# Performance work log

Measured on AMD Instinct MI355X. Metric: run time of the kernel, lower is better.

## Reference

```python
import jax, jax.numpy as jnp
import numpy as np

H, L, NB = 128, 2048, 64  # features, seq len, half state size (conj-symmetric N=128)


def _forward(u, x_re, x_im, Lambda_re, Lambda_im, B_re, B_im, C_re, C_im, D, d):
    Lam = (Lambda_re + 1j * Lambda_im).astype(jnp.complex64)   # (H, NB) discrete diag A
    B = (B_re + 1j * B_im).astype(jnp.complex64)               # (H, NB)
    C = (C_re + 1j * C_im).astype(jnp.complex64)               # (H, NB)
    x0 = (x_re + 1j * x_im).astype(jnp.complex64)              # (H, NB) initial state
    Hn, Ln = u.shape
    # scan elements (A_t, b_t, d_t); identity element (1, x0, False) prepended at t=0
    A = jnp.concatenate([jnp.ones((Hn, 1, NB), jnp.complex64),
                         jnp.broadcast_to(Lam[:, None, :], (Hn, Ln, NB))], axis=1)
    b = jnp.concatenate([x0[:, None, :],
                         B[:, None, :] * u[:, :, None].astype(jnp.complex64)], axis=1)
    dd = jnp.concatenate([jnp.zeros((1,), bool), d.astype(bool)])[None, :, None]  # (1, L+1, 1)

    def combine(lhs, rhs):
        # reset-aware associative combine: if right done-flag set, drop left contribution
        A_i, b_i, c_i = lhs
        A_j, b_j, c_j = rhs
        return (jnp.where(c_j, A_j, A_j * A_i),
                jnp.where(c_j, b_j, A_j * b_i + b_j),
                jnp.logical_or(c_i, c_j))

    _, xs, _ = jax.lax.associative_scan(combine, (A, b, dd), axis=1)
    xs = xs[:, 1:]                                             # (H, L, NB) hidden states
    # conj symmetry: y_t = 2*Re(C @ x_t) + D * u_t
    y = 2.0 * jnp.real(jnp.einsum('hn,hln->hl', C, xs)) + D[:, None] * u
    return y, xs[:, -1]


def setup_inputs():
    key = jax.random.key(0)
    ks = jax.random.split(key, 8)
    # stable ZOH-discretized HiPPO-like diagonal system (mirrors LSSL-f init)
    dts = jnp.logspace(-3.0, -1.0, H)                          # (H,) per-feature timescales
    k = jnp.arange(NB, dtype=jnp.float32)
    lam_c = -0.5 + 1j * jnp.pi * (2.0 * k + 1.0)               # (NB,) continuous poles
    lam_d = jnp.exp(dts[:, None] * lam_c[None, :]).astype(jnp.complex64)  # (H, NB), |.|<1
    Bc = ((jax.random.normal(ks[0], (NB,)) + 1j * jax.random.normal(ks[1], (NB,)))
          / jnp.sqrt(2.0 * NB)).astype(jnp.complex64)
    Bd = (((lam_d - 1.0) / lam_c[None, :]) * Bc[None, :]).astype(jnp.complex64)  # (H, NB)
    C = ((jax.random.normal(ks[2], (H, NB)) + 1j * jax.random.normal(ks[3], (H, NB)))
         / jnp.sqrt(float(NB))).astype(jnp.complex64)
    return {
        "u": jax.random.normal(ks[4], (H, L), jnp.float32),
        "x_re": jnp.zeros((H, NB), jnp.float32),
        "x_im": jnp.zeros((H, NB), jnp.float32),
        "Lambda_re": jnp.real(lam_d).astype(jnp.float32),
        "Lambda_im": jnp.imag(lam_d).astype(jnp.float32),
        "B_re": jnp.real(Bd).astype(jnp.float32),
        "B_im": jnp.imag(Bd).astype(jnp.float32),
        "C_re": jnp.real(C).astype(jnp.float32),
        "C_im": jnp.imag(C).astype(jnp.float32),
        "D": jax.random.normal(ks[5], (H,), jnp.float32),
        "d": jax.random.bernoulli(ks[6], 0.01, (L,)),
    }


def reference(u, x_re, x_im, Lambda_re, Lambda_im, B_re, B_im, C_re, C_im, D, d):
    return _forward(u, x_re, x_im, Lambda_re, Lambda_im, B_re, B_im, C_re, C_im, D, d)
```

## Files before the change

### kernel.cpp

```cpp
#include <hip/hip_runtime.h>

#define Hn 128
#define Ln 2048
#define NBn 64
#define K 64
#define G 32
#define PITCH 65

__global__ __launch_bounds__(64) void phase1_local(
    const float* __restrict__ u,
    const float* __restrict__ Lre,  const float* __restrict__ Lim,
    const float* __restrict__ Bre,  const float* __restrict__ Bim,
    const float* __restrict__ Cre,  const float* __restrict__ Cim,
    const float* __restrict__ Dv,   const int* __restrict__ dflag,
    float* __restrict__ out,
    float* __restrict__ Acr, float* __restrict__ Aci,
    float* __restrict__ Bcr, float* __restrict__ Bci)
{
    __shared__ float g_s[K * PITCH];
    __shared__ float u_s[K];
    __shared__ int   d_s[K];

    const int g = blockIdx.x, h = blockIdx.y, n = threadIdx.x;
    const int hn = h * NBn + n;
    const int l0 = g * K;

    const float lre = Lre[hn], lim = Lim[hn];
    const float bre = Bre[hn], bim = Bim[hn];
    const float c2re =  2.0f * Cre[hn];
    const float c2im = -2.0f * Cim[hn];
    const float Dh   = Dv[h];

    u_s[n] = u[h * Ln + l0 + n];
    const int dn = dflag[l0 + n];
    d_s[n] = dn;
    __syncthreads();

    float zre = 0.f, zim = 0.f;
    #pragma unroll
    for (int k = 0; k < K; ++k) {
        const float ul = u_s[k];
        const bool  rs = d_s[k] != 0;
        const float bur = bre * ul;
        const float bui = bim * ul;
        const float tre = fmaf(lre, zre, fmaf(-lim, zim, bur));
        const float tim = fmaf(lre, zim, fmaf( lim, zre, bui));
        zre = rs ? bur : tre;
        zim = rs ? bui : tim;
        g_s[k * PITCH + n] = fmaf(c2re, zre, c2im * zim);
    }
    __syncthreads();

    const float* row = g_s + n * PITCH;
    float a0 = 0.f, a1 = 0.f, a2 = 0.f, a3 = 0.f;
    #pragma unroll
    for (int k = 0; k < NBn; k += 4) {
        a0 += row[k + 0]; a1 += row[k + 1];
        a2 += row[k + 2]; a3 += row[k + 3];
    }
    out[h * Ln + l0 + n] = (a0 + a1) + (a2 + a3) + Dh * u_s[n];

    const unsigned long long bal = __ballot(dn != 0);
    float pr = lre, pi = lim;
    #pragma unroll
    for (int it = 0; it < 6; ++it) {
        const float nr = pr * pr - pi * pi;
        const float ni = 2.f * pr * pi;
        pr = nr; pi = ni;
    }
    if (bal) { pr = 0.f; pi = 0.f; }
    const int idx = (h * G + g) * NBn + n;
    Acr[idx] = pr;  Aci[idx] = pi;
    Bcr[idx] = zre; Bci[idx] = zim;
}

__global__ __launch_bounds__(64) void phase2_combine(
    const float* __restrict__ x_re, const float* __restrict__ x_im,
    const float* __restrict__ Acr,  const float* __restrict__ Aci,
    float* __restrict__ Bcr,        float* __restrict__ Bci,
    float* __restrict__ out)
{
    const int h = blockIdx.x, n = threadIdx.x;
    const int hn = h * NBn + n;
    float sre = x_re[hn], sim = x_im[hn];
    #pragma unroll
    for (int g = 0; g < G; ++g) {
        const int idx = (h * G + g) * NBn + n;
        const float ar = Acr[idx], ai = Aci[idx];
        const float br = Bcr[idx], bi = Bci[idx];
        Bcr[idx] = sre;
        Bci[idx] = sim;
        const float nr = fmaf(ar, sre, fmaf(-ai, sim, br));
        const float ni = fmaf(ar, sim, fmaf( ai, sre, bi));
        sre = nr; sim = ni;
    }
    float* xlast = out + Hn * Ln;
    xlast[2 * hn + 0] = sre;
    xlast[2 * hn + 1] = sim;
}

__global__ __launch_bounds__(64) void phase3_fixup(
    const float* __restrict__ Lre, const float* __restrict__ Lim,
    const float* __restrict__ Cre, const float* __restrict__ Cim,
    const int* __restrict__ dflag,
    const float* __restrict__ Scr, const float* __restrict__ Sci,
    float* __restrict__ out)
{
    __shared__ float g_s[K * PITCH];

    const int g = blockIdx.x, h = blockIdx.y, n = threadIdx.x;
    const int hn = h * NBn + n;
    const int l0 = g * K;
    const int idx = (h * G + g) * NBn + n;

    const float sr = Scr[idx], si = Sci[idx];
    const float cr = Cre[hn],  ci = Cim[hn];
    const float lre = Lre[hn], lim = Lim[hn];

    float tr = cr * sr - ci * si;
    float ti = cr * si + ci * sr;

    const int dn = dflag[l0 + n];
    const unsigned long long bal = __ballot(dn != 0);
    const int kr = bal ? (__ffsll(bal) - 1) : K;

    #pragma unroll
    for (int k = 0; k < K; ++k) {
        const float nr = fmaf(lre, tr, -lim * ti);
        const float ni = fmaf(lre, ti,  lim * tr);
        tr = nr; ti = ni;
        g_s[k * PITCH + n] = tr;
    }
    __syncthreads();

    const float* row = g_s + n * PITCH;
    float a0 = 0.f, a1 = 0.f, a2 = 0.f, a3 = 0.f;
    #pragma unroll
    for (int k = 0; k < NBn; k += 4) {
        a0 += row[k + 0]; a1 += row[k + 1];
        a2 += row[k + 2]; a3 += row[k + 3];
    }
    if (n < kr)
        out[h * Ln + l0 + n] += 2.f * ((a0 + a1) + (a2 + a3));
}

extern "C" void kernel_launch(void* const* d_in, const int* in_sizes, int n_in,
                              void* d_out, int out_size, void* d_ws, size_t ws_size,
                              hipStream_t stream) {
    const float* u    = (const float*)d_in[0];
    const float* x_re = (const float*)d_in[1];
    const float* x_im = (const float*)d_in[2];
    const float* Lre  = (const float*)d_in[3];
    const float* Lim  = (const float*)d_in[4];
    const float* Bre  = (const float*)d_in[5];
    const float* Bim  = (const float*)d_in[6];
    const float* Cre  = (const float*)d_in[7];
    const float* Cim  = (const float*)d_in[8];
    const float* Dv   = (const float*)d_in[9];
    const int*   dfl  = (const int*)d_in[10];
    float* out = (float*)d_out;

    const int HGN = Hn * G * NBn;
    float* Acr = (float*)d_ws;
    float* Aci = Acr + HGN;
    float* Bcr = Aci + HGN;
    float* Bci = Bcr + HGN;

    dim3 gridA(G, Hn);
    phase1_local<<<gridA, 64, 0, stream>>>(u, Lre, Lim, Bre, Bim, Cre, Cim,
                                           Dv, dfl, out, Acr, Aci, Bcr, Bci);
    phase2_combine<<<Hn, 64, 0, stream>>>(x_re, x_im, Acr, Aci, Bcr, Bci, out);
    phase3_fixup<<<gridA, 64, 0, stream>>>(Lre, Lim, Cre, Cim, dfl,
                                           Bcr, Bci, out);
}
```

Before: 91.00 us.

## Fuse carry-combine into fixup kernel and vectorize shared-memory reductions

Drops the separate serial combine kernel. Each fixup block recomputes its own incoming carry state by folding the chunk summaries before it, which removes one launch and the global write/read of carries. The power recurrence in the fixup is split into two interleaved chains using lambda squared to shorten the dependency chain. The reset flags become a wave ballot bitmask instead of a shared array, and the row reductions use float4 loads with pitch 68. In exchange, later blocks do redundant serial work of up to 31 steps, and the padding change may reintroduce bank conflicts on the column writes.

```diff
diff --git a/kernel.cpp b/kernel.cpp
--- a/kernel.cpp
+++ b/kernel.cpp
@@ -5,7 +5,7 @@
 #define NBn 64
 #define K 64
 #define G 32
-#define PITCH 65
+#define PITCH 68
 
 __global__ __launch_bounds__(64) void phase1_local(
     const float* __restrict__ u,
@@ -19,7 +19,6 @@
 {
     __shared__ float g_s[K * PITCH];
     __shared__ float u_s[K];
-    __shared__ int   d_s[K];
 
     const int g = blockIdx.x, h = blockIdx.y, n = threadIdx.x;
     const int hn = h * NBn + n;
@@ -33,77 +32,54 @@
 
     u_s[n] = u[h * Ln + l0 + n];
     const int dn = dflag[l0 + n];
-    d_s[n] = dn;
+    const unsigned long long m = __ballot(dn != 0);
     __syncthreads();
 
     float zre = 0.f, zim = 0.f;
     #pragma unroll
     for (int k = 0; k < K; ++k) {
-        const float ul = u_s[k];
-        const bool  rs = d_s[k] != 0;
+        const bool  rs  = (m >> k) & 1ull;
+        const float ul  = u_s[k];
+        const float lrk = rs ? 0.f : lre;
+        const float lik = rs ? 0.f : lim;
         const float bur = bre * ul;
         const float bui = bim * ul;
-        const float tre = fmaf(lre, zre, fmaf(-lim, zim, bur));
-        const float tim = fmaf(lre, zim, fmaf( lim, zre, bui));
-        zre = rs ? bur : tre;
-        zim = rs ? bui : tim;
+        const float nr = fmaf(lrk, zre, fmaf(-lik, zim, bur));
+        const float ni = fmaf(lrk, zim, fmaf( lik, zre, bui));
+        zre = nr; zim = ni;
         g_s[k * PITCH + n] = fmaf(c2re, zre, c2im * zim);
     }
     __syncthreads();
 
-    const float* row = g_s + n * PITCH;
+    const float4* row4 = reinterpret_cast<const float4*>(g_s + n * PITCH);
     float a0 = 0.f, a1 = 0.f, a2 = 0.f, a3 = 0.f;
     #pragma unroll
-    for (int k = 0; k < NBn; k += 4) {
-        a0 += row[k + 0]; a1 += row[k + 1];
-        a2 += row[k + 2]; a3 += row[k + 3];
+    for (int k = 0; k < NBn / 4; ++k) {
+        const float4 v = row4[k];
+        a0 += v.x; a1 += v.y; a2 += v.z; a3 += v.w;
     }
     out[h * Ln + l0 + n] = (a0 + a1) + (a2 + a3) + Dh * u_s[n];
 
-    const unsigned long long bal = __ballot(dn != 0);
     float pr = lre, pi = lim;
     #pragma unroll
     for (int it = 0; it < 6; ++it) {
-        const float nr = pr * pr - pi * pi;
-        const float ni = 2.f * pr * pi;
-        pr = nr; pi = ni;
+        const float sr2 = pr * pr - pi * pi;
+        const float si2 = 2.f * pr * pi;
+        pr = sr2; pi = si2;
     }
-    if (bal) { pr = 0.f; pi = 0.f; }
+    if (m) { pr = 0.f; pi = 0.f; }
     const int idx = (h * G + g) * NBn + n;
     Acr[idx] = pr;  Aci[idx] = pi;
     Bcr[idx] = zre; Bci[idx] = zim;
 }
 
-__global__ __launch_bounds__(64) void phase2_combine(
+__global__ __launch_bounds__(64) void phase23_fixup(
     const float* __restrict__ x_re, const float* __restrict__ x_im,
+    const float* __restrict__ Lre,  const float* __restrict__ Lim,
+    const float* __restrict__ Cre,  const float* __restrict__ Cim,
+    const int* __restrict__ dflag,
     const float* __restrict__ Acr,  const float* __restrict__ Aci,
-    float* __restrict__ Bcr,        float* __restrict__ Bci,
-    float* __restrict__ out)
-{
-    const int h = blockIdx.x, n = threadIdx.x;
-    const int hn = h * NBn + n;
-    float sre = x_re[hn], sim = x_im[hn];
-    #pragma unroll
-    for (int g = 0; g < G; ++g) {
-        const int idx = (h * G + g) * NBn + n;
-        const float ar = Acr[idx], ai = Aci[idx];
-        const float br = Bcr[idx], bi = Bci[idx];
-        Bcr[idx] = sre;
-        Bci[idx] = sim;
-        const float nr = fmaf(ar, sre, fmaf(-ai, sim, br));
-        const float ni = fmaf(ar, sim, fmaf( ai, sre, bi));
-        sre = nr; sim = ni;
-    }
-    float* xlast = out + Hn * Ln;
-    xlast[2 * hn + 0] = sre;
-    xlast[2 * hn + 1] = sim;
-}
-
-__global__ __launch_bounds__(64) void phase3_fixup(
-    const float* __restrict__ Lre, const float* __restrict__ Lim,
-    const float* __restrict__ Cre, const float* __restrict__ Cim,
-    const int* __restrict__ dflag,
-    const float* __restrict__ Scr, const float* __restrict__ Sci,
+    const float* __restrict__ Bcr,  const float* __restrict__ Bci,
     float* __restrict__ out)
 {
     __shared__ float g_s[K * PITCH];
@@ -111,34 +87,65 @@
     const int g = blockIdx.x, h = blockIdx.y, n = threadIdx.x;
     const int hn = h * NBn + n;
     const int l0 = g * K;
-    const int idx = (h * G + g) * NBn + n;
 
-    const float sr = Scr[idx], si = Sci[idx];
-    const float cr = Cre[hn],  ci = Cim[hn];
+    float sre = x_re[hn], sim = x_im[hn];
+    for (int j = 0; j < g; ++j) {
+        const int idx = (h * G + j) * NBn + n;
+        const float ar = Acr[idx], ai = Aci[idx];
+        const float br = Bcr[idx], bi = Bci[idx];
+        const float nr = fmaf(ar, sre, fmaf(-ai, sim, br));
+        const float ni = fmaf(ar, sim, fmaf( ai, sre, bi));
+        sre = nr; sim = ni;
+    }
+
+    if (g == G - 1) {
+        const int idx = (h * G + g) * NBn + n;
+        const float ar = Acr[idx], ai = Aci[idx];
+        const float br = Bcr[idx], bi = Bci[idx];
+        const float fr = fmaf(ar, sre, fmaf(-ai, sim, br));
+        const float fi = fmaf(ar, sim, fmaf( ai, sre, bi));
+        float* xlast = out + Hn * Ln;
+        xlast[2 * hn + 0] = fr;
+        xlast[2 * hn + 1] = fi;
+    }
+
+    const float cr = Cre[hn], ci = Cim[hn];
     const float lre = Lre[hn], lim = Lim[hn];
-
-    float tr = cr * sr - ci * si;
-    float ti = cr * si + ci * sr;
 
     const int dn = dflag[l0 + n];
     const unsigned long long bal = __ballot(dn != 0);
     const int kr = bal ? (__ffsll(bal) - 1) : K;
 
+    const float pr = cr * sre - ci * sim;
+    const float pi = cr * sim + ci * sre;
+    const float l2r = lre * lre - lim * lim;
+    const float l2i = 2.f * lre * lim;
+
+    float tAr = fmaf(lre, pr, -lim * pi);
+    float tAi = fmaf(lre, pi,  lim * pr);
+    float tBr = fmaf(l2r, pr, -l2i * pi);
+    float tBi = fmaf(l2r, pi,  l2i * pr);
+    g_s[0 * PITCH + n] = tAr;
+    g_s[1 * PITCH + n] = tBr;
     #pragma unroll
-    for (int k = 0; k < K; ++k) {
-        const float nr = fmaf(lre, tr, -lim * ti);
-        const float ni = fmaf(lre, ti,  lim * tr);
-        tr = nr; ti = ni;
-        g_s[k * PITCH + n] = tr;
+    for (int k = 2; k < K; k += 2) {
+        const float nAr = fmaf(l2r, tAr, -l2i * tAi);
+        const float nAi = fmaf(l2r, tAi,  l2i * tAr);
+        tAr = nAr; tAi = nAi;
+        g_s[k * PITCH + n] = tAr;
+        const float nBr = fmaf(l2r, tBr, -l2i * tBi);
+        const float nBi = fmaf(l2r, tBi,  l2i * tBr);
+        tBr = nBr; tBi = nBi;
+        g_s[(k + 1) * PITCH + n] = tBr;
     }
     __syncthreads();
 
-    const float* row = g_s + n * PITCH;
+    const float4* row4 = reinterpret_cast<const float4*>(g_s + n * PITCH);
     float a0 = 0.f, a1 = 0.f, a2 = 0.f, a3 = 0.f;
     #pragma unroll
-    for (int k = 0; k < NBn; k += 4) {
-        a0 += row[k + 0]; a1 += row[k + 1];
-        a2 += row[k + 2]; a3 += row[k + 3];
+    for (int k = 0; k < NBn / 4; ++k) {
+        const float4 v = row4[k];
+        a0 += v.x; a1 += v.y; a2 += v.z; a3 += v.w;
     }
     if (n < kr)
         out[h * Ln + l0 + n] += 2.f * ((a0 + a1) + (a2 + a3));
@@ -166,10 +173,9 @@
     float* Bcr = Aci + HGN;
     float* Bci = Bcr + HGN;
 
-    dim3 gridA(G, Hn);
-    phase1_local<<<gridA, 64, 0, stream>>>(u, Lre, Lim, Bre, Bim, Cre, Cim,
-                                           Dv, dfl, out, Acr, Aci, Bcr, Bci);
-    phase2_combine<<<Hn, 64, 0, stream>>>(x_re, x_im, Acr, Aci, Bcr, Bci, out);
-    phase3_fixup<<<gridA, 64, 0, stream>>>(Lre, Lim, Cre, Cim, dfl,
-                                           Bcr, Bci, out);
+    dim3 grid(G, Hn);
+    phase1_local<<<grid, 64, 0, stream>>>(u, Lre, Lim, Bre, Bim, Cre, Cim,
+                                          Dv, dfl, out, Acr, Aci, Bcr, Bci);
+    phase23_fixup<<<grid, 64, 0, stream>>>(x_re, x_im, Lre, Lim, Cre, Cim,
+                                           dfl, Acr, Aci, Bcr, Bci, out);
 }
```

After: 112.2 us. +23.3%, slower.
